# Kernel tuning notes

Hardware: AMD Instinct MI355X
Metric: run time of the kernel (lower is better)

## Reference

```python
import jax, jax.numpy as jnp
import numpy as np

POOLING_RATE = 4
K = 16  # neighbor_num
EPS = 1e-5


def setup_inputs() -> dict:
    key = jax.random.key(0)
    ks = jax.random.split(key, 20)
    B, N, C, D = 8, 4096, 256, 64
    inp = {
        'vertices': jax.random.normal(ks[0], (B, 3, N), jnp.float32),
        'feature_map': jax.random.normal(ks[1], (B, C, N), jnp.float32),
        # pos_mlp: Conv2d(3,64) -> BN(64) -> LeakyReLU -> Conv2d(64,C)
        'pw1': jax.random.normal(ks[2], (64, 3), jnp.float32) * 0.2,
        'pb1': jax.random.normal(ks[3], (64,), jnp.float32) * 0.02,
        'bn1_g': 1.0 + 0.1 * jax.random.normal(ks[4], (64,), jnp.float32),
        'bn1_b': 0.02 * jax.random.normal(ks[5], (64,), jnp.float32),
        'bn1_m': 0.02 * jax.random.normal(ks[6], (64,), jnp.float32),
        'bn1_v': jnp.ones((64,), jnp.float32),
        'pw2': jax.random.normal(ks[7], (C, 64), jnp.float32) * 0.1,
        'pb2': jax.random.normal(ks[8], (C,), jnp.float32) * 0.02,
        # attn_mlp: Conv2d(C,D) -> BN(D) -> LeakyReLU -> Conv2d(D, 3+C)
        'aw1': jax.random.normal(ks[9], (D, C), jnp.float32) * 0.05,
        'ab1': jax.random.normal(ks[10], (D,), jnp.float32) * 0.02,
        'bn2_g': 1.0 + 0.1 * jax.random.normal(ks[11], (D,), jnp.float32),
        'bn2_b': 0.02 * jax.random.normal(ks[12], (D,), jnp.float32),
        'bn2_m': 0.02 * jax.random.normal(ks[13], (D,), jnp.float32),
        'bn2_v': jnp.ones((D,), jnp.float32),
        'aw2': jax.random.normal(ks[14], (3 + C, D), jnp.float32) * 0.1,
        'ab2': jax.random.normal(ks[15], (3 + C,), jnp.float32) * 0.02,
    }
    return inp


def _fps(xyz, npoint):
    # xyz: [B,N,3] -> indices [B,npoint], deterministic start at index 0
    B, N, _ = xyz.shape

    def body(carry, _):
        dist, far = carry
        centroid = jnp.take_along_axis(xyz, far[:, None, None], axis=1)  # [B,1,3]
        d = jnp.sum((xyz - centroid) ** 2, axis=-1)  # [B,N]
        dist = jnp.minimum(dist, d)
        nxt = jnp.argmax(dist, axis=1).astype(jnp.int32)
        return (dist, nxt), far

    init = (jnp.full((B, N), 1e10, xyz.dtype), jnp.zeros((B,), jnp.int32))
    _, idxs = jax.lax.scan(body, init, None, length=npoint)
    return idxs.T  # [B, npoint]


def _conv1x1(x, w, b):
    # x: [B,Cin,M,K], w: [Cout,Cin]
    return jnp.einsum('oc,bcmk->bomk', w, x) + b[None, :, None, None]


def _bn(x, g, b, m, v):
    s = g / jnp.sqrt(v + EPS)
    return (x - m[None, :, None, None]) * s[None, :, None, None] + b[None, :, None, None]


def _forward(vertices, feature_map, pw1, pb1, bn1_g, bn1_b, bn1_m, bn1_v, pw2, pb2,
             aw1, ab1, bn2_g, bn2_b, bn2_m, bn2_v, aw2, ab2):
    B, _, N = vertices.shape
    M = int(N / POOLING_RATE + 0.5)
    xyz = jnp.transpose(vertices, (0, 2, 1))  # [B,N,3]

    fps_idx = _fps(xyz, M)  # [B,M]
    key_point = jnp.take_along_axis(vertices, fps_idx[:, None, :], axis=2)      # [B,3,M]
    key_feat = jnp.take_along_axis(feature_map, fps_idx[:, None, :], axis=2)    # [B,C,M]

    # kNN of key points in full cloud: squared distances [B,M,N]
    key_xyz = jnp.transpose(key_point, (0, 2, 1))  # [B,M,3]
    sqr = (jnp.sum(key_xyz ** 2, -1)[:, :, None]
           + jnp.sum(xyz ** 2, -1)[:, None, :]
           - 2.0 * jnp.einsum('bmc,bnc->bmn', key_xyz, xyz))
    _, knn_idx = jax.lax.top_k(-sqr, K)  # [B,M,K]

    gather = jax.vmap(lambda v, i: v[:, i])  # v:[C,N], i:[M,K] -> [C,M,K]
    group_point = gather(vertices, knn_idx)     # [B,3,M,K]
    group_feat = gather(feature_map, knn_idx)   # [B,C,M,K]

    qk_rel = key_feat[:, :, :, None] - group_feat   # [B,C,M,K]
    pos_rel = key_point[:, :, :, None] - group_point  # [B,3,M,K]

    h = jax.nn.leaky_relu(_bn(_conv1x1(pos_rel, pw1, pb1), bn1_g, bn1_b, bn1_m, bn1_v), 0.2)
    pos_embedding = _conv1x1(h, pw2, pb2)  # [B,C,M,K]

    h2 = jax.nn.leaky_relu(_bn(_conv1x1(qk_rel + pos_embedding, aw1, ab1),
                               bn2_g, bn2_b, bn2_m, bn2_v), 0.2)
    sample_weight = jax.nn.softmax(_conv1x1(h2, aw2, ab2), axis=-1)  # [B,3+C,M,K]

    new_xyz_w = sample_weight[:, :3]
    new_feat_w = sample_weight[:, 3:]
    group_feat = group_feat + pos_embedding
    new_feat = jnp.einsum('bcmk,bcmk->bcm', new_feat_w, group_feat)   # [B,C,M]
    new_point = jnp.einsum('bcmk,bcmk->bcm', new_xyz_w, group_point)  # [B,3,M]
    # concatenate (new_point, new_feat) along channel for a single output
    return jnp.concatenate([new_point, new_feat], axis=1)  # [B,3+C,M]


def reference(vertices, feature_map, pw1, pb1, bn1_g, bn1_b, bn1_m, bn1_v, pw2, pb2,
              aw1, ab1, bn2_g, bn2_b, bn2_m, bn2_v, aw2, ab2):
    return _forward(vertices, feature_map, pw1, pb1, bn1_g, bn1_b, bn1_m, bn1_v, pw2, pb2,
                    aw1, ab1, bn2_g, bn2_b, bn2_m, bn2_v, aw2, ab2)
```

## Files before the change

### kernel.cpp

```cpp
#include <hip/hip_runtime.h>
#include <math.h>

#define BB 8
#define NN 4096
#define CC 256
#define DD 64
#define MM 1024
#define KNB 16
#define OC 259
#define CHUNK 128
#define NCHUNK 8

typedef unsigned long long ull;

#define GRID_MAIN 1544
#define GRID_AUX 2585
#define AUX_G2 512

__device__ __forceinline__ void g2_unit(
    int u, int tid, char* smem, const float* fm, const float* aw1,
    const float* g2v, const float* v2, float* G2) {
  float (*a_l)[68] = (float(*)[68])smem;
  float (*b_l)[68] = (float(*)[68])(smem + 64 * 68 * 4);
  int b = u >> 6;
  int n0 = (u & 63) * 64;
  int rr = tid >> 4, q4 = tid & 15;
  float s2v[4];
#pragma unroll
  for (int j = 0; j < 4; ++j)
    s2v[j] = g2v[q4 * 4 + j] * rsqrtf(v2[q4 * 4 + j] + 1e-5f);
  float acc[4][4];
#pragma unroll
  for (int q = 0; q < 4; ++q)
#pragma unroll
    for (int x = 0; x < 4; ++x) acc[q][x] = 0.f;
  for (int c0 = 0; c0 < 256; c0 += 64) {
    __syncthreads();
#pragma unroll
    for (int rep = 0; rep < 4; ++rep) {
      int cc = rr + rep * 16;
      *(float4*)&a_l[cc][q4 * 4] =
          *(const float4*)&fm[((size_t)b * CC + c0 + cc) * NN + n0 + q4 * 4];
      float bv[4];
#pragma unroll
      for (int j = 0; j < 4; ++j)
        bv[j] = aw1[(q4 * 4 + j) * 256 + c0 + cc] * s2v[j];
      *(float4*)&b_l[cc][q4 * 4] = make_float4(bv[0], bv[1], bv[2], bv[3]);
    }
    __syncthreads();
#pragma unroll 8
    for (int kk = 0; kk < 64; ++kk) {
      float4 a4 = *(const float4*)&a_l[kk][rr * 4];
      float4 b4 = *(const float4*)&b_l[kk][q4 * 4];
      float av[4] = {a4.x, a4.y, a4.z, a4.w};
#pragma unroll
      for (int q = 0; q < 4; ++q) {
        acc[q][0] += av[q] * b4.x;
        acc[q][1] += av[q] * b4.y;
        acc[q][2] += av[q] * b4.z;
        acc[q][3] += av[q] * b4.w;
      }
    }
  }
#pragma unroll
  for (int q = 0; q < 4; ++q)
    *(float4*)&G2[((size_t)b * NN + n0 + rr * 4 + q) * 64 + q4 * 4] =
        make_float4(acc[q][0], acc[q][1], acc[q][2], acc[q][3]);
}

__device__ __forceinline__ void prep_unit(
    int tid, const float* pw1, const float* pb1, const float* g1,
    const float* bb1, const float* m1, const float* v1, const float* pw2,
    const float* aw1, const float* g2v, const float* bb2, const float* m2,
    const float* v2, const float* aw2, const float* ab1, float* w1f,
    float* b1f, float* ab1f, float* pw2t, float* aw1t, float* aw2t) {
  if (tid < 64) {
    float s = g1[tid] * rsqrtf(v1[tid] + 1e-5f);
    w1f[tid * 4 + 0] = pw1[tid * 3 + 0] * s;
    w1f[tid * 4 + 1] = pw1[tid * 3 + 1] * s;
    w1f[tid * 4 + 2] = pw1[tid * 3 + 2] * s;
    w1f[tid * 4 + 3] = 0.f;
    b1f[tid] = (pb1[tid] - m1[tid]) * s + bb1[tid];
    float s2 = g2v[tid] * rsqrtf(v2[tid] + 1e-5f);
    ab1f[tid] = (ab1[tid] - m2[tid]) * s2 + bb2[tid];
  }
  for (int x = tid; x < 64 * 256; x += 256) {
    int i = x >> 8, c = x & 255;
    pw2t[x] = pw2[c * 64 + i];
  }
  for (int x = tid; x < 256 * 64; x += 256) {
    int c = x >> 6, d = x & 63;
    float s2 = g2v[d] * rsqrtf(v2[d] + 1e-5f);
    aw1t[x] = aw1[d * 256 + c] * s2;
  }
  for (int x = tid; x < 64 * OC; x += 256) {
    int i = x / OC, o = x % OC;
    aw2t[i * 260 + o] = aw2[o * 64 + i];
  }
}

__device__ __forceinline__ void w12_unit(
    int w, int tid, const float* pw2, const float* aw1, const float* g2v,
    const float* v2, float* W12t) {
  int i = tid & 63;
  int d = w * 4 + (tid >> 6);
  float s2 = g2v[d] * rsqrtf(v2[d] + 1e-5f);
  const float* arow = aw1 + d * 256;
  float s = 0.f;
#pragma unroll 4
  for (int c = 0; c < 256; ++c) s += pw2[c * 64 + i] * arow[c];
  W12t[i * 64 + d] = s * s2;
}

__device__ __forceinline__ void transpose_unit(
    int rb, int tid, char* smem, const float* fm, float* fm_t) {
  float (*tile)[65] = (float(*)[65])smem;
  int b = rb >> 8;
  int rem = rb & 255;
  int c0 = (rem >> 6) * 64;
  int n0 = (rem & 63) * 64;
  const float* src = fm + (size_t)b * CC * NN;
  float* dst = fm_t + (size_t)b * NN * CC;
  int tx = tid & 63, ty = tid >> 6;
  for (int r = ty; r < 64; r += 4)
    tile[r][tx] = src[(size_t)(c0 + r) * NN + n0 + tx];
  __syncthreads();
  for (int r = ty; r < 64; r += 4)
    dst[(size_t)(n0 + r) * CC + c0 + tx] = tile[tx][r];
}

__device__ __forceinline__ void knn_item(
    int b, int m, int lane, float* dbuf, const float* verts,
    const int* fpsi, int* knni) {
  const float* vb = verts + (size_t)b * 3 * NN;
  int jm = fpsi[b * MM + m];
  float kx = vb[jm], ky = vb[NN + jm], kz = vb[2 * NN + jm];
  float kn = kx * kx + ky * ky + kz * kz;
  float v1 = INFINITY, v2 = INFINITY;
  int i1 = -1, i2 = -1;
  for (int t = 0; t < 64; ++t) {
    int j = t * 64 + lane;
    float x = vb[j], y = vb[NN + j], z = vb[2 * NN + j];
    float xn = x * x + y * y + z * z;
    float d = kn + xn - 2.0f * (kx * x + ky * y + kz * z);
    dbuf[lane * 65 + t] = d;
    if (d < v1) { v2 = v1; i2 = i1; v1 = d; i1 = j; }
    else if (d < v2) { v2 = d; i2 = j; }
  }
  for (int it = 0; it < KNB; ++it) {
    float rv = v1;
    int ri = i1;
#pragma unroll
    for (int off = 32; off >= 1; off >>= 1) {
      float ov = __shfl_down(rv, off, 64);
      int oi = __shfl_down(ri, off, 64);
      if (ov < rv || (ov == rv && oi < ri)) { rv = ov; ri = oi; }
    }
    ri = __shfl(ri, 0, 64);
    if (lane == 0) knni[(size_t)(b * MM + m) * KNB + it] = ri;
    if (i1 == ri) {
      dbuf[lane * 65 + (ri >> 6)] = INFINITY;
      v1 = v2; i1 = i2;
      v2 = INFINITY; i2 = -1;
      if (i1 < 0) {
        v1 = INFINITY; v2 = INFINITY; i1 = -1; i2 = -1;
        for (int t = 0; t < 64; ++t) {
          float d = dbuf[lane * 65 + t];
          int j = t * 64 + lane;
          if (d < v1) { v2 = v1; i2 = i1; v1 = d; i1 = j; }
          else if (d < v2) { v2 = d; i2 = j; }
        }
      }
    }
  }
}

struct FuseS {
  float W12_l[64][68];
  float h_l[16][68];
  float hT_l[64][20];
  float h2T_l[64][20];
  float vmp[4][64];
  float vm_l[64];
  float kfpb[256];
  float pb2_l[256];
  float gp[3][16];
  float kp[4];
  int kidx[16];
};

__device__ __forceinline__ void fuse_item(
    int b, int m, int tid, char* smem, const float* verts,
    const float* fm_t, const float* G2, const int* fpsi, const int* knni,
    const float* w1f, const float* b1f, const float* ab1f,
    const float* aw1t, const float* W12t, const float* pw2t,
    const float* pb2, const float* aw2t, const float* ab2, float* out) {
  FuseS* S = (FuseS*)smem;
  const float* vb = verts + (size_t)b * 3 * NN;
  const float* fb = fm_t + (size_t)b * NN * CC;
  int jm = fpsi[b * MM + m];
  if (tid < 16) S->kidx[tid] = knni[((size_t)b * MM + m) * 16 + tid];
  S->kfpb[tid] = fb[(size_t)jm * CC + tid] + pb2[tid];
  S->pb2_l[tid] = pb2[tid];
  if (tid < 3) S->kp[tid] = vb[tid * NN + jm];
  __syncthreads();

  if (tid < 48) {
    int c = tid >> 4, k = tid & 15;
    S->gp[c][k] = vb[c * NN + S->kidx[k]];
  }
  {
    int i = tid >> 4, d4 = tid & 15;
#pragma unroll
    for (int rep = 0; rep < 4; ++rep)
      *(float4*)&S->W12_l[i + rep * 16][d4 * 4] =
          *(const float4*)&W12t[(i + rep * 16) * 64 + d4 * 4];
  }
  {
    int d = tid & 63, part = tid >> 6;
    float acc = 0.f;
#pragma unroll 4
    for (int cc = 0; cc < 64; ++cc) {
      int c = part * 64 + cc;
      acc += aw1t[c * 64 + d] * S->kfpb[c];
    }
    S->vmp[part][d] = acc;
  }
  __syncthreads();
  if (tid < 64)
    S->vm_l[tid] = S->vmp[0][tid] + S->vmp[1][tid] + S->vmp[2][tid] +
                   S->vmp[3][tid] + ab1f[tid];

  {
    int d = tid & 63, part = tid >> 6;
    float wd0 = w1f[d * 4 + 0], wd1 = w1f[d * 4 + 1], wd2 = w1f[d * 4 + 2];
    float bd = b1f[d];
#pragma unroll
    for (int j = 0; j < 4; ++j) {
      int k = part * 4 + j;
      float hv = wd0 * (S->kp[0] - S->gp[0][k]) +
                 wd1 * (S->kp[1] - S->gp[1][k]) +
                 wd2 * (S->kp[2] - S->gp[2][k]) + bd;
      hv = (hv > 0.f) ? hv : 0.2f * hv;
      S->h_l[k][d] = hv;
      S->hT_l[d][k] = hv;
    }
  }
  __syncthreads();

  {
    int k = tid & 15, d2 = tid >> 4;
    float4 g4 =
        *(const float4*)&G2[((size_t)b * NN + S->kidx[k]) * 64 + d2 * 4];
    float a0 = 0.f, a1 = 0.f, a2 = 0.f, a3 = 0.f;
#pragma unroll 4
    for (int i = 0; i < 64; ++i) {
      float hv = S->h_l[k][i];
      float4 w4 = *(const float4*)&S->W12_l[i][d2 * 4];
      a0 += hv * w4.x; a1 += hv * w4.y; a2 += hv * w4.z; a3 += hv * w4.w;
    }
    float4 v4 = *(const float4*)&S->vm_l[d2 * 4];
    float r0 = v4.x - g4.x + a0;
    float r1 = v4.y - g4.y + a1;
    float r2 = v4.z - g4.z + a2;
    float r3 = v4.w - g4.w + a3;
    S->h2T_l[d2 * 4 + 0][k] = (r0 > 0.f) ? r0 : 0.2f * r0;
    S->h2T_l[d2 * 4 + 1][k] = (r1 > 0.f) ? r1 : 0.2f * r1;
    S->h2T_l[d2 * 4 + 2][k] = (r2 > 0.f) ? r2 : 0.2f * r2;
    S->h2T_l[d2 * 4 + 3][k] = (r3 > 0.f) ? r3 : 0.2f * r3;
  }
  __syncthreads();

  if (tid < 3) {
    float lg[16];
    float bias = ab2[tid];
#pragma unroll
    for (int k = 0; k < 16; ++k) lg[k] = bias;
    const float* wp = aw2t + tid;
    for (int i = 0; i < 64; ++i) {
      float wv = wp[i * 260];
      float4 ha = *(const float4*)&S->h2T_l[i][0];
      float4 hb = *(const float4*)&S->h2T_l[i][4];
      float4 hc = *(const float4*)&S->h2T_l[i][8];
      float4 hd = *(const float4*)&S->h2T_l[i][12];
      lg[0] += wv * ha.x;  lg[1] += wv * ha.y;  lg[2] += wv * ha.z;  lg[3] += wv * ha.w;
      lg[4] += wv * hb.x;  lg[5] += wv * hb.y;  lg[6] += wv * hb.z;  lg[7] += wv * hb.w;
      lg[8] += wv * hc.x;  lg[9] += wv * hc.y;  lg[10] += wv * hc.z; lg[11] += wv * hc.w;
      lg[12] += wv * hd.x; lg[13] += wv * hd.y; lg[14] += wv * hd.z; lg[15] += wv * hd.w;
    }
    float mx = lg[0];
#pragma unroll
    for (int k = 1; k < 16; ++k) mx = fmaxf(mx, lg[k]);
    float sum = 0.f;
#pragma unroll
    for (int k = 0; k < 16; ++k) { lg[k] = __expf(lg[k] - mx); sum += lg[k]; }
    float inv = 1.f / sum;
    float a2 = 0.f;
#pragma unroll
    for (int k = 0; k < 16; ++k) a2 += lg[k] * S->gp[tid][k];
    out[((size_t)b * OC + tid) * MM + m] = a2 * inv;
  }

  {
    int o = tid + 3;
    float gfv[16];
#pragma unroll
    for (int k = 0; k < 16; ++k)
      gfv[k] = fb[(size_t)S->kidx[k] * CC + tid];
    float lg[16];
    float bias = ab2[o];
#pragma unroll
    for (int k = 0; k < 16; ++k) lg[k] = bias;
    const float* wp = aw2t + o;
#pragma unroll 4
    for (int i = 0; i < 64; ++i) {
      float wv = wp[i * 260];
      float4 ha = *(const float4*)&S->h2T_l[i][0];
      float4 hb = *(const float4*)&S->h2T_l[i][4];
      float4 hc = *(const float4*)&S->h2T_l[i][8];
      float4 hd = *(const float4*)&S->h2T_l[i][12];
      lg[0] += wv * ha.x;  lg[1] += wv * ha.y;  lg[2] += wv * ha.z;  lg[3] += wv * ha.w;
      lg[4] += wv * hb.x;  lg[5] += wv * hb.y;  lg[6] += wv * hb.z;  lg[7] += wv * hb.w;
      lg[8] += wv * hc.x;  lg[9] += wv * hc.y;  lg[10] += wv * hc.z; lg[11] += wv * hc.w;
      lg[12] += wv * hd.x; lg[13] += wv * hd.y; lg[14] += wv * hd.z; lg[15] += wv * hd.w;
    }
    float mx = lg[0];
#pragma unroll
    for (int k = 1; k < 16; ++k) mx = fmaxf(mx, lg[k]);
    float sum = 0.f;
#pragma unroll
    for (int k = 0; k < 16; ++k) { lg[k] = __expf(lg[k] - mx); sum += lg[k]; }
    float inv = 1.f / sum;
#pragma unroll
    for (int k = 0; k < 16; ++k) lg[k] *= inv;
    float acc = 0.f;
#pragma unroll
    for (int k = 0; k < 16; ++k) acc += lg[k] * gfv[k];
    const float* pcol = pw2t + tid;
#pragma unroll 4
    for (int i = 0; i < 64; ++i) {
      float p = pcol[i * 256];
      float4 ha = *(const float4*)&S->hT_l[i][0];
      float4 hb = *(const float4*)&S->hT_l[i][4];
      float4 hc = *(const float4*)&S->hT_l[i][8];
      float4 hd = *(const float4*)&S->hT_l[i][12];
      float hw = lg[0] * ha.x + lg[1] * ha.y + lg[2] * ha.z + lg[3] * ha.w +
                 lg[4] * hb.x + lg[5] * hb.y + lg[6] * hb.z + lg[7] * hb.w +
                 lg[8] * hc.x + lg[9] * hc.y + lg[10] * hc.z + lg[11] * hc.w +
                 lg[12] * hd.x + lg[13] * hd.y + lg[14] * hd.z + lg[15] * hd.w;
      acc += p * hw;
    }
    out[((size_t)b * OC + o) * MM + m] = S->pb2_l[tid] + acc;
  }
}

__global__ __launch_bounds__(256, 3) void pipe(
    const float* __restrict__ verts, const float* __restrict__ fm,
    const float* __restrict__ pw1, const float* __restrict__ pb1,
    const float* __restrict__ g1, const float* __restrict__ bb1,
    const float* __restrict__ m1, const float* __restrict__ v1,
    const float* __restrict__ pw2, const float* __restrict__ pb2,
    const float* __restrict__ aw1, const float* __restrict__ ab1,
    const float* __restrict__ g2v, const float* __restrict__ bb2,
    const float* __restrict__ m2, const float* __restrict__ v2,
    const float* __restrict__ aw2, const float* __restrict__ ab2,
    float* __restrict__ fm_t, float* __restrict__ G2,
    int* __restrict__ fpsi, int* __restrict__ knni,
    float* __restrict__ w1f, float* __restrict__ b1f,
    float* __restrict__ ab1f, float* __restrict__ pw2t,
    float* __restrict__ aw1t, float* __restrict__ aw2t,
    float* __restrict__ W12t, float* __restrict__ dstate,
    int* __restrict__ fstate, float* __restrict__ out,
    int c_fps, int c_knn, int c_fuse, int aux_flag) {
  __shared__ __align__(16) char smem[49728];
  int blk = blockIdx.x;
  int tid = threadIdx.x;

  if (blk < 8) {
    if (c_fps < 0) return;
    float* lx = (float*)smem;
    float* ly = lx + NN;
    float* lz = ly + NN;
    ull* wres = (ull*)(lz + NN);
    int* fps_l = (int*)(wres + 8);
    int b = blk;
    const float* vb = verts + (size_t)b * 3 * NN;
    float px[16], py[16], pz[16], dist[16];
#pragma unroll
    for (int r = 0; r < 16; ++r) {
      int j = tid + r * 256;
      px[r] = vb[j]; py[r] = vb[NN + j]; pz[r] = vb[2 * NN + j];
      lx[j] = px[r]; ly[j] = py[r]; lz[j] = pz[r];
    }
    int far;
    if (c_fps == 0) {
#pragma unroll
      for (int r = 0; r < 16; ++r) dist[r] = 1e10f;
      far = 0;
    } else {
#pragma unroll
      for (int r = 0; r < 16; ++r)
        dist[r] = dstate[(size_t)b * NN + tid + r * 256];
      far = fstate[b];
    }
    __syncthreads();
    int s0 = c_fps * CHUNK, s1 = s0 + CHUNK;
    for (int s = s0; s < s1; ++s) {
      if (tid == 0) fps_l[s - s0] = far;
      if (s == MM - 1) break;
      float cx = lx[far], cy = ly[far], cz = lz[far];
      float vmax = -1.0f;
#pragma unroll
      for (int r = 0; r < 16; ++r) {
        float dx = px[r] - cx, dy = py[r] - cy, dz = pz[r] - cz;
        float d = dx * dx + dy * dy + dz * dz;
        dist[r] = fminf(dist[r], d);
        vmax = fmaxf(vmax, dist[r]);
      }
#define VRED(CTRL)                                                            \
      {                                                                       \
        int o = __builtin_amdgcn_update_dpp(__float_as_int(vmax),             \
                                            __float_as_int(vmax), CTRL, 0xF,  \
                                            0xF, false);                      \
        vmax = fmaxf(vmax, __int_as_float(o));                                \
      }
      VRED(0x111) VRED(0x112) VRED(0x114) VRED(0x118) VRED(0x142) VRED(0x143)
#undef VRED
      float svmax =
          __int_as_float(__builtin_amdgcn_readlane(__float_as_int(vmax), 63));
      int minj = 0x7FFFFFFF;
#pragma unroll
      for (int r = 0; r < 16; ++r) {
        int cand = (dist[r] == svmax) ? (tid + r * 256) : 0x7FFFFFFF;
        minj = (cand < minj) ? cand : minj;
      }
#define IRED(CTRL)                                                            \
      {                                                                       \
        int o = __builtin_amdgcn_update_dpp(minj, minj, CTRL, 0xF, 0xF,       \
                                            false);                          \
        minj = (o < minj) ? o : minj;                                         \
      }
      IRED(0x111) IRED(0x112) IRED(0x114) IRED(0x118) IRED(0x142) IRED(0x143)
#undef IRED
      if ((tid & 63) == 63)
        wres[(s & 1) * 4 + (tid >> 6)] =
            ((ull)(unsigned)__float_as_int(svmax) << 12) |
            (ull)(4095 - minj);
      __syncthreads();
      int p = s & 1;
      ull k0 = wres[p * 4 + 0], k1 = wres[p * 4 + 1];
      ull k2 = wres[p * 4 + 2], k3 = wres[p * 4 + 3];
      ull a = (k0 > k1) ? k0 : k1;
      ull c = (k2 > k3) ? k2 : k3;
      a = (c > a) ? c : a;
      far = 4095 - (int)(a & 0xFFFull);
    }
    __syncthreads();
    for (int x = tid; x < CHUNK; x += 256) fpsi[b * MM + s0 + x] = fps_l[x];
    if (s1 < MM) {
#pragma unroll
      for (int r = 0; r < 16; ++r)
        dstate[(size_t)b * NN + tid + r * 256] = dist[r];
      if (tid == 0) fstate[b] = far;
    }
    return;
  }

  if (aux_flag) {
    int u = blk - 8;
    if (u < AUX_G2) {
      g2_unit(u, tid, smem, fm, aw1, g2v, v2, G2);
    } else if (u == AUX_G2) {
      prep_unit(tid, pw1, pb1, g1, bb1, m1, v1, pw2, aw1, g2v, bb2, m2, v2,
                aw2, ab1, w1f, b1f, ab1f, pw2t, aw1t, aw2t);
    } else if (u < AUX_G2 + 17) {
      w12_unit(u - (AUX_G2 + 1), tid, pw2, aw1, g2v, v2, W12t);
    } else {
      transpose_unit(u - (AUX_G2 + 17), tid, smem, fm, fm_t);
    }
    return;
  }

  if (blk < 520) {
    if (c_knn < 0) return;
    int wave = tid >> 6, lane = tid & 63;
    if (wave >= 2) return;
    int item = (blk - 8) * 2 + wave;
    int b = item >> 7;
    int m = c_knn * CHUNK + (item & 127);
    float* dbuf = (float*)smem + wave * (64 * 65);
    knn_item(b, m, lane, dbuf, verts, fpsi, knni);
    return;
  }

  {
    if (c_fuse < 0) return;
    int e = blk - 520;
    int b = e & 7;
    int m = c_fuse * CHUNK + (e >> 3);
    fuse_item(b, m, tid, smem, verts, fm_t, G2, fpsi, knni, w1f, b1f, ab1f,
              aw1t, W12t, pw2t, pb2, aw2t, ab2, out);
  }
}

extern "C" void kernel_launch(void* const* d_in, const int* in_sizes, int n_in,
                              void* d_out, int out_size, void* d_ws,
                              size_t ws_size, hipStream_t stream) {
  (void)in_sizes; (void)n_in; (void)out_size; (void)ws_size;
  const float* verts = (const float*)d_in[0];
  const float* fm = (const float*)d_in[1];
  const float* pw1 = (const float*)d_in[2];
  const float* pb1 = (const float*)d_in[3];
  const float* g1 = (const float*)d_in[4];
  const float* bb1 = (const float*)d_in[5];
  const float* m1 = (const float*)d_in[6];
  const float* v1 = (const float*)d_in[7];
  const float* pw2 = (const float*)d_in[8];
  const float* pb2 = (const float*)d_in[9];
  const float* aw1 = (const float*)d_in[10];
  const float* ab1 = (const float*)d_in[11];
  const float* g2 = (const float*)d_in[12];
  const float* bb2 = (const float*)d_in[13];
  const float* m2 = (const float*)d_in[14];
  const float* v2 = (const float*)d_in[15];
  const float* aw2 = (const float*)d_in[16];
  const float* ab2 = (const float*)d_in[17];
  float* out = (float*)d_out;

  char* ws = (char*)d_ws;
  float* fm_t = (float*)ws;
  float* G2 = (float*)(ws + 33554432);
  int* fpsi = (int*)(ws + 41943040);
  int* knni = (int*)(ws + 41975808);
  float* w1f = (float*)(ws + 42500096);
  float* b1f = w1f + 256;
  float* ab1f = b1f + 64;
  float* pw2t = ab1f + 64;
  float* aw1t = pw2t + 64 * 256;
  float* aw2t = aw1t + 256 * 64;
  float* W12t = aw2t + 64 * 260;
  float* dstate = (float*)(ws + 42715648);
  int* fstate = (int*)(ws + 42846720);

#define LAUNCH(grid, cf, ck, cz, ax)                                          \
  hipLaunchKernelGGL(pipe, dim3(grid), dim3(256), 0, stream, verts, fm, pw1,  \
                     pb1, g1, bb1, m1, v1, pw2, pb2, aw1, ab1, g2, bb2, m2,   \
                     v2, aw2, ab2, fm_t, G2, fpsi, knni, w1f, b1f, ab1f,      \
                     pw2t, aw1t, aw2t, W12t, dstate, fstate, out, cf, ck, cz, \
                     ax)

  LAUNCH(GRID_AUX, 0, -1, -1, 1);
  LAUNCH(GRID_MAIN, 1, 0, -1, 0);
  LAUNCH(GRID_MAIN, 2, 1, 0, 0);
  LAUNCH(GRID_MAIN, 3, 2, 1, 0);
  LAUNCH(GRID_MAIN, 4, 3, 2, 0);
  LAUNCH(GRID_MAIN, 5, 4, 3, 0);
  LAUNCH(GRID_MAIN, 6, 5, 4, 0);
  LAUNCH(GRID_MAIN, 7, 6, 5, 0);
  LAUNCH(GRID_MAIN, -1, 7, 6, 0);
  LAUNCH(GRID_MAIN, -1, -1, 7, 0);
#undef LAUNCH
}
```

Before: 926.8 us.

## Fuse KNN search into fuse blocks and drop the separate KNN pipeline stage

KNN selection now runs inside each fuse block: the first wave computes the 16 nearest neighbours into LDS, reusing the W12_l shared-memory region as scratch, before the fuse computation starts. This removes the KNN block range, the global knni buffer and one launch from the chunked pipeline. It cuts global index traffic and shortens the pipeline, but KNN now sits on the critical path of each fuse block, with three of four waves idle during the search.

```diff
diff --git a/kernel.cpp b/kernel.cpp
--- a/kernel.cpp
+++ b/kernel.cpp
@@ -13,7 +13,7 @@
 
 typedef unsigned long long ull;
 
-#define GRID_MAIN 1544
+#define GRID_MAIN 1032
 #define GRID_AUX 2585
 #define AUX_G2 512
 
@@ -129,9 +129,9 @@
     dst[(size_t)(n0 + r) * CC + c0 + tx] = tile[tx][r];
 }
 
-__device__ __forceinline__ void knn_item(
+__device__ __forceinline__ void knn_to_lds(
     int b, int m, int lane, float* dbuf, const float* verts,
-    const int* fpsi, int* knni) {
+    const int* fpsi, int* kidx) {
   const float* vb = verts + (size_t)b * 3 * NN;
   int jm = fpsi[b * MM + m];
   float kx = vb[jm], ky = vb[NN + jm], kz = vb[2 * NN + jm];
@@ -157,7 +157,7 @@
       if (ov < rv || (ov == rv && oi < ri)) { rv = ov; ri = oi; }
     }
     ri = __shfl(ri, 0, 64);
-    if (lane == 0) knni[(size_t)(b * MM + m) * KNB + it] = ri;
+    if (lane == 0) kidx[it] = ri;
     if (i1 == ri) {
       dbuf[lane * 65 + (ri >> 6)] = INFINITY;
       v1 = v2; i1 = i2;
@@ -191,15 +191,19 @@
 
 __device__ __forceinline__ void fuse_item(
     int b, int m, int tid, char* smem, const float* verts,
-    const float* fm_t, const float* G2, const int* fpsi, const int* knni,
+    const float* fm_t, const float* G2, const int* fpsi,
     const float* w1f, const float* b1f, const float* ab1f,
     const float* aw1t, const float* W12t, const float* pw2t,
     const float* pb2, const float* aw2t, const float* ab2, float* out) {
   FuseS* S = (FuseS*)smem;
   const float* vb = verts + (size_t)b * 3 * NN;
   const float* fb = fm_t + (size_t)b * NN * CC;
+
+  if (tid < 64)
+    knn_to_lds(b, m, tid, (float*)S->W12_l, verts, fpsi, S->kidx);
+  __syncthreads();
+
   int jm = fpsi[b * MM + m];
-  if (tid < 16) S->kidx[tid] = knni[((size_t)b * MM + m) * 16 + tid];
   S->kfpb[tid] = fb[(size_t)jm * CC + tid] + pb2[tid];
   S->pb2_l[tid] = pb2[tid];
   if (tid < 3) S->kp[tid] = vb[tid * NN + jm];
@@ -365,13 +369,13 @@
     const float* __restrict__ m2, const float* __restrict__ v2,
     const float* __restrict__ aw2, const float* __restrict__ ab2,
     float* __restrict__ fm_t, float* __restrict__ G2,
-    int* __restrict__ fpsi, int* __restrict__ knni,
+    int* __restrict__ fpsi,
     float* __restrict__ w1f, float* __restrict__ b1f,
     float* __restrict__ ab1f, float* __restrict__ pw2t,
     float* __restrict__ aw1t, float* __restrict__ aw2t,
     float* __restrict__ W12t, float* __restrict__ dstate,
     int* __restrict__ fstate, float* __restrict__ out,
-    int c_fps, int c_knn, int c_fuse, int aux_flag) {
+    int c_fps, int c_fuse, int aux_flag) {
   __shared__ __align__(16) char smem[49728];
   int blk = blockIdx.x;
   int tid = threadIdx.x;
@@ -481,24 +485,12 @@
     return;
   }
 
-  if (blk < 520) {
-    if (c_knn < 0) return;
-    int wave = tid >> 6, lane = tid & 63;
-    if (wave >= 2) return;
-    int item = (blk - 8) * 2 + wave;
-    int b = item >> 7;
-    int m = c_knn * CHUNK + (item & 127);
-    float* dbuf = (float*)smem + wave * (64 * 65);
-    knn_item(b, m, lane, dbuf, verts, fpsi, knni);
-    return;
-  }
-
   {
     if (c_fuse < 0) return;
-    int e = blk - 520;
+    int e = blk - 8;
     int b = e & 7;
     int m = c_fuse * CHUNK + (e >> 3);
-    fuse_item(b, m, tid, smem, verts, fm_t, G2, fpsi, knni, w1f, b1f, ab1f,
+    fuse_item(b, m, tid, smem, verts, fm_t, G2, fpsi, w1f, b1f, ab1f,
               aw1t, W12t, pw2t, pb2, aw2t, ab2, out);
   }
 }
@@ -531,7 +523,6 @@
   float* fm_t = (float*)ws;
   float* G2 = (float*)(ws + 33554432);
   int* fpsi = (int*)(ws + 41943040);
-  int* knni = (int*)(ws + 41975808);
   float* w1f = (float*)(ws + 42500096);
   float* b1f = w1f + 256;
   float* ab1f = b1f + 64;
@@ -542,22 +533,20 @@
   float* dstate = (float*)(ws + 42715648);
   int* fstate = (int*)(ws + 42846720);
 
-#define LAUNCH(grid, cf, ck, cz, ax)                                          \
+#define LAUNCH(grid, cf, cz, ax)                                              \
   hipLaunchKernelGGL(pipe, dim3(grid), dim3(256), 0, stream, verts, fm, pw1,  \
                      pb1, g1, bb1, m1, v1, pw2, pb2, aw1, ab1, g2, bb2, m2,   \
-                     v2, aw2, ab2, fm_t, G2, fpsi, knni, w1f, b1f, ab1f,      \
-                     pw2t, aw1t, aw2t, W12t, dstate, fstate, out, cf, ck, cz, \
-                     ax)
-
-  LAUNCH(GRID_AUX, 0, -1, -1, 1);
-  LAUNCH(GRID_MAIN, 1, 0, -1, 0);
-  LAUNCH(GRID_MAIN, 2, 1, 0, 0);
-  LAUNCH(GRID_MAIN, 3, 2, 1, 0);
-  LAUNCH(GRID_MAIN, 4, 3, 2, 0);
-  LAUNCH(GRID_MAIN, 5, 4, 3, 0);
-  LAUNCH(GRID_MAIN, 6, 5, 4, 0);
-  LAUNCH(GRID_MAIN, 7, 6, 5, 0);
-  LAUNCH(GRID_MAIN, -1, 7, 6, 0);
-  LAUNCH(GRID_MAIN, -1, -1, 7, 0);
+                     v2, aw2, ab2, fm_t, G2, fpsi, w1f, b1f, ab1f,            \
+                     pw2t, aw1t, aw2t, W12t, dstate, fstate, out, cf, cz, ax)
+
+  LAUNCH(GRID_AUX, 0, -1, 1);
+  LAUNCH(GRID_MAIN, 1, 0, 0);
+  LAUNCH(GRID_MAIN, 2, 1, 0);
+  LAUNCH(GRID_MAIN, 3, 2, 0);
+  LAUNCH(GRID_MAIN, 4, 3, 0);
+  LAUNCH(GRID_MAIN, 5, 4, 0);
+  LAUNCH(GRID_MAIN, 6, 5, 0);
+  LAUNCH(GRID_MAIN, 7, 6, 0);
+  LAUNCH(GRID_MAIN, -1, 7, 0);
 #undef LAUNCH
 }
```

Result: slower. 1.012 ms (+9.2%).
